# Kernel tuning notes

Hardware: AMD Instinct MI355X
Metric: run time of the kernel (lower is better)

Reference implementation:

```python
import jax, jax.numpy as jnp
import numpy as np

EPSILON = 1e-5  # parameters.EPSILON
BN_EPS = 1e-5
N_NODES, N_EDGES, D = 50000, 400000, 128


def batch_norm(x, gamma, beta):
    # BatchNorm1d in training mode: biased batch statistics over dim 0
    m = jnp.mean(x, axis=0)
    v = jnp.var(x, axis=0)
    return (x - m) * jax.lax.rsqrt(v + BN_EPS) * gamma + beta


def setup_inputs() -> dict:
    key = jax.random.key(0)
    ks = jax.random.split(key, 16)
    s = 0.05
    d = D
    inp = {
        "h": jax.random.normal(ks[0], (N_NODES, d), jnp.float32),
        "e": jax.random.normal(ks[1], (N_EDGES, d), jnp.float32),
        "src": jax.random.randint(ks[2], (N_EDGES,), 0, N_NODES, jnp.int32),
        "dst": jax.random.randint(ks[3], (N_EDGES,), 0, N_NODES, jnp.int32),
        # weights stored [in, out]
        "W_emb_node": jax.random.normal(ks[4], (d, d)) * s,
        "W_emb_edge": jax.random.normal(ks[5], (d, d)) * s,
        "W_emb_eta": jax.random.normal(ks[6], (d, d)) * s,
        "Uw": jax.random.normal(ks[7], (d, d)) * s, "Ub": jnp.zeros((d,)),
        "Vw": jax.random.normal(ks[8], (d, d)) * s, "Vb": jnp.zeros((d,)),
        "W1w": jax.random.normal(ks[9], (d, d)) * s, "W1b": jnp.zeros((d,)),
        "W2w": jax.random.normal(ks[10], (d, d)) * s, "W2b": jnp.zeros((d,)),
        "W3w": jax.random.normal(ks[11], (d, d)) * s, "W3b": jnp.zeros((d,)),
        "h_gamma": jnp.ones((d,)), "h_beta": jnp.zeros((d,)),
        "e_gamma": jnp.ones((d,)), "e_beta": jnp.zeros((d,)),
    }
    return inp


def reference(h, e, src, dst, W_emb_node, W_emb_edge, W_emb_eta,
              Uw, Ub, Vw, Vb, W1w, W1b, W2w, W2b, W3w, W3b,
              h_gamma, h_beta, e_gamma, e_beta):
    n_nodes = h.shape[0]
    # node-level linear projections
    h_emb = h @ W_emb_node                 # [N, d]
    Uh = h @ Uw + Ub                       # [N, d]
    Vh = h @ Vw + Vb                       # [N, d]
    W2h = h @ W2w + W2b                    # [N, d]
    W3h = h @ W3w + W3b                    # [N, d]
    # edge-level
    e_emb = e @ W_emb_edge                 # [E, d]
    W1e = e @ W1w + W1b                    # [E, d]
    # edge update: e_ij = emb(e) + ReLU(BN(W1 e + W2 h_src + W3 h_dst))
    pre_e = W1e + W2h[src] + W3h[dst]      # gather [E, d]
    e_new = e_emb + jax.nn.relu(batch_norm(pre_e, e_gamma, e_beta))
    # gate: sigma_ij = embedding_eta(sigmoid(e_ij))
    sigma = jax.nn.sigmoid(e_new) @ W_emb_eta  # [E, d]
    # weighted-sum aggregation to destination nodes
    num = jax.ops.segment_sum(sigma * Vh[src], dst, num_segments=n_nodes)
    den = jax.ops.segment_sum(sigma, dst, num_segments=n_nodes)
    agg = num / (den + EPSILON)            # [N, d]
    h_new = h_emb + jax.nn.relu(batch_norm(Uh + agg, h_gamma, h_beta))
    return (h_new, e_new)
```

## Files before the change

kernel.cpp:

```cpp
#include <hip/hip_runtime.h>
#include <cstdint>
#include <cstddef>
#include <cmath>

#define DD 128

typedef short bf16x8 __attribute__((ext_vector_type(8)));
typedef float f32x4 __attribute__((ext_vector_type(4)));

static __device__ __forceinline__ short f2bf(float f){
  union { float f; uint32_t u; } v; v.f = f;
  uint32_t r = v.u + 0x7FFFu + ((v.u >> 16) & 1u);
  return (short)(r >> 16);
}
static __device__ __forceinline__ float bf2f(short h){
  union { uint32_t u; float f; } v; v.u = ((uint32_t)(uint16_t)h) << 16;
  return v.f;
}
static __device__ __forceinline__ double shfl_xor_f64(double v, int m){
  long long l = __double_as_longlong(v);
  int lo = (int)(l & 0xffffffffLL);
  int hi = (int)((unsigned long long)l >> 32);
  lo = __shfl_xor(lo, m, 64);
  hi = __shfl_xor(hi, m, 64);
  return __longlong_as_double(((long long)hi << 32) | (unsigned long long)(unsigned int)lo);
}

template<int EP>
__global__ __launch_bounds__(256, 2) void fgemm_k(
    const float* __restrict__ X, const float* __restrict__ W,
    const float* __restrict__ bias, float* __restrict__ Y,
    int M, int nTiles,
    const int* __restrict__ src, const int* __restrict__ dst,
    const float* __restrict__ T2, const float* __restrict__ T3,
    double* __restrict__ eSum, double* __restrict__ eSumSq)
{
  __shared__ float sA[128][36];
  __shared__ float sW[32][128];
  __shared__ double redS[(EP == 1) ? 4 : 1][32][4];
  __shared__ double redQ[(EP == 1) ? 4 : 1][32][4];

  const int tid = threadIdx.x, tx = tid & 31, ty = tid >> 5;
  const int c0 = tx * 4, r0 = ty * 16;
  const int lane = tid & 63, wv = tid >> 6;
  const int sa_r = tid >> 1, sa_k = (tid & 1) * 16;
  const int sw_k = tid >> 3, sw_c = (tid & 7) * 16;

  float bias_c[4];
  #pragma unroll
  for (int j = 0; j < 4; ++j) bias_c[j] = bias ? bias[c0 + j] : 0.0f;

  double st_s[4] = {0,0,0,0}, st_q[4] = {0,0,0,0};

  #pragma unroll 1
  for (int tile = blockIdx.x; tile < nTiles; tile += gridDim.x){
    const int rowBase = tile * 128;
    float acc[16][4];
    #pragma unroll
    for (int r = 0; r < 16; ++r)
      #pragma unroll
      for (int j = 0; j < 4; ++j) acc[r][j] = 0.0f;

    #pragma unroll 1
    for (int h = 0; h < 4; ++h){
      {
        const float* wp = W + (size_t)(h*32 + sw_k) * DD + sw_c;
        #pragma unroll
        for (int i = 0; i < 4; ++i)
          *(f32x4*)&sW[sw_k][sw_c + i*4] = *(const f32x4*)(wp + i*4);
      }
      {
        int ar = rowBase + sa_r; if (ar >= M) ar = M - 1;
        const float* xp = X + (size_t)ar * DD + h*32 + sa_k;
        #pragma unroll
        for (int i = 0; i < 4; ++i)
          *(f32x4*)&sA[sa_r][sa_k + i*4] = *(const f32x4*)(xp + i*4);
      }
      __syncthreads();

      #pragma unroll
      for (int q = 0; q < 8; ++q){
        f32x4 b0 = *(const f32x4*)&sW[4*q + 0][c0];
        f32x4 b1 = *(const f32x4*)&sW[4*q + 1][c0];
        f32x4 b2 = *(const f32x4*)&sW[4*q + 2][c0];
        f32x4 b3 = *(const f32x4*)&sW[4*q + 3][c0];
        #pragma unroll
        for (int r = 0; r < 16; ++r){
          f32x4 a = *(const f32x4*)&sA[r0 + r][4*q];
          #pragma unroll
          for (int j = 0; j < 4; ++j){
            float t = acc[r][j];
            t = fmaf(a[0], b0[j], t); t = fmaf(a[1], b1[j], t);
            t = fmaf(a[2], b2[j], t); t = fmaf(a[3], b3[j], t);
            acc[r][j] = t;
          }
        }
      }
      __syncthreads();
    }

    #pragma unroll
    for (int r = 0; r < 16; ++r){
      int row = rowBase + r0 + r;
      if (row < M){
        size_t base = (size_t)row * DD + c0;
        if (EP == 0){
          f32x4 o;
          #pragma unroll
          for (int j = 0; j < 4; ++j) o[j] = acc[r][j] + bias_c[j];
          *(f32x4*)&Y[base] = o;
        } else {
          int s = src[row], d = dst[row];
          f32x4 t2 = *(const f32x4*)&T2[(size_t)s * DD + c0];
          f32x4 t3 = *(const f32x4*)&T3[(size_t)d * DD + c0];
          f32x4 o;
          #pragma unroll
          for (int j = 0; j < 4; ++j){
            o[j] = ((acc[r][j] + bias_c[j]) + t2[j]) + t3[j];
            st_s[j] += (double)o[j];
            st_q[j] += (double)o[j] * (double)o[j];
          }
          *(f32x4*)&Y[base] = o;
        }
      }
    }
  }

  if (EP == 1){
    #pragma unroll
    for (int j = 0; j < 4; ++j){
      st_s[j] += shfl_xor_f64(st_s[j], 32);
      st_q[j] += shfl_xor_f64(st_q[j], 32);
    }
    if (lane < 32){
      #pragma unroll
      for (int j = 0; j < 4; ++j){ redS[wv][lane][j] = st_s[j]; redQ[wv][lane][j] = st_q[j]; }
    }
    __syncthreads();
    if (tid < 128){
      int txx = tid >> 2, j = tid & 3;
      double s = 0.0, q = 0.0;
      #pragma unroll
      for (int w = 0; w < 4; ++w){ s += redS[w][txx][j]; q += redQ[w][txx][j]; }
      atomicAdd(&eSum[txx*4 + j], s);
      atomicAdd(&eSumSq[txx*4 + j], q);
    }
  }
}

__global__ __launch_bounds__(256, 2) void psgemm_k(
    const float* __restrict__ preE, const float* __restrict__ eEmb,
    const float* __restrict__ Weta,
    float* __restrict__ eNew, float* __restrict__ sigmaOut,
    const float* __restrict__ mF, const float* __restrict__ rF,
    const float* __restrict__ gF, const float* __restrict__ bF,
    int M, int nTiles)
{
  __shared__ float sA[128][36];
  __shared__ float sW[32][128];
  __shared__ float sBN[4][128];

  const int tid = threadIdx.x, tx = tid & 31, ty = tid >> 5;
  const int c0 = tx * 4, r0 = ty * 16;
  const int sa_r = tid >> 1, sa_k = (tid & 1) * 16;
  const int sw_k = tid >> 3, sw_c = (tid & 7) * 16;

  if (tid < 128){
    sBN[0][tid] = mF[tid]; sBN[1][tid] = rF[tid];
    sBN[2][tid] = gF[tid]; sBN[3][tid] = bF[tid];
  }
  __syncthreads();

  #pragma unroll 1
  for (int tile = blockIdx.x; tile < nTiles; tile += gridDim.x){
    const int rowBase = tile * 128;
    const int ar = rowBase + sa_r;

    float acc[16][4];
    #pragma unroll
    for (int r = 0; r < 16; ++r)
      #pragma unroll
      for (int j = 0; j < 4; ++j) acc[r][j] = 0.0f;

    #pragma unroll 1
    for (int h = 0; h < 4; ++h){
      {
        const float* wp = Weta + (size_t)(h*32 + sw_k) * DD + sw_c;
        #pragma unroll
        for (int i = 0; i < 4; ++i)
          *(f32x4*)&sW[sw_k][sw_c + i*4] = *(const f32x4*)(wp + i*4);
      }
      {
        int gcb = h*32 + sa_k;
        const float* pp = preE + (size_t)ar * DD + gcb;
        const float* ep = eEmb + (size_t)ar * DD + gcb;
        float* np = eNew + (size_t)ar * DD + gcb;
        #pragma unroll
        for (int i = 0; i < 4; ++i){
          f32x4 pe = *(const f32x4*)(pp + i*4);
          f32x4 em = *(const f32x4*)(ep + i*4);
          f32x4 mm = *(const f32x4*)&sBN[0][gcb + i*4];
          f32x4 rr = *(const f32x4*)&sBN[1][gcb + i*4];
          f32x4 gg = *(const f32x4*)&sBN[2][gcb + i*4];
          f32x4 bb = *(const f32x4*)&sBN[3][gcb + i*4];
          f32x4 en, sg;
          #pragma unroll
          for (int j = 0; j < 4; ++j){
            float xm  = pe[j] - mm[j];
            float t1  = xm * rr[j];
            float t2v = t1 * gg[j];
            float t3v = t2v + bb[j];
            float t = fmaxf(t3v, 0.0f);
            en[j] = em[j] + t;
            sg[j] = 1.0f / (1.0f + expf(-en[j]));
          }
          *(f32x4*)(np + i*4) = en;
          *(f32x4*)&sA[sa_r][sa_k + i*4] = sg;
        }
      }
      __syncthreads();

      #pragma unroll
      for (int q = 0; q < 8; ++q){
        f32x4 b0 = *(const f32x4*)&sW[4*q + 0][c0];
        f32x4 b1 = *(const f32x4*)&sW[4*q + 1][c0];
        f32x4 b2 = *(const f32x4*)&sW[4*q + 2][c0];
        f32x4 b3 = *(const f32x4*)&sW[4*q + 3][c0];
        #pragma unroll
        for (int r = 0; r < 16; ++r){
          f32x4 a = *(const f32x4*)&sA[r0 + r][4*q];
          #pragma unroll
          for (int j = 0; j < 4; ++j){
            float t = acc[r][j];
            t = fmaf(a[0], b0[j], t); t = fmaf(a[1], b1[j], t);
            t = fmaf(a[2], b2[j], t); t = fmaf(a[3], b3[j], t);
            acc[r][j] = t;
          }
        }
      }
      __syncthreads();
    }

    #pragma unroll
    for (int r = 0; r < 16; ++r){
      int row = rowBase + r0 + r;
      f32x4 o;
      #pragma unroll
      for (int j = 0; j < 4; ++j) o[j] = acc[r][j];
      *(f32x4*)&sigmaOut[(size_t)row * DD + c0] = o;
    }
  }
}

__global__ void hist_k(const int* __restrict__ dst, int NE, int* __restrict__ counts){
  int i = blockIdx.x * blockDim.x + threadIdx.x;
  if (i < NE) atomicAdd(&counts[dst[i]], 1);
}

__global__ __launch_bounds__(1024, 1) void scan_k(const int* __restrict__ counts, int NN,
                                                  int* __restrict__ rowStart, int* __restrict__ cursor){
  __shared__ int part[1024];
  const int T = 1024, t = threadIdx.x;
  const int chunk = (NN + T - 1) / T;
  const int lo = t * chunk;
  const int hi = (lo + chunk < NN) ? lo + chunk : NN;
  int s = 0;
  for (int i = lo; i < hi; ++i) s += counts[i];
  part[t] = s;
  __syncthreads();
  for (int off = 1; off < T; off <<= 1){
    int v = (t >= off) ? part[t - off] : 0;
    __syncthreads();
    part[t] += v;
    __syncthreads();
  }
  int run = (t == 0) ? 0 : part[t - 1];
  for (int i = lo; i < hi; ++i){ rowStart[i] = run; cursor[i] = run; run += counts[i]; }
  if (t == T - 1) rowStart[NN] = run;
}

__global__ void place_k(const int* __restrict__ dst, int NE,
                        int* __restrict__ cursor, int* __restrict__ edgeIdx){
  int i = blockIdx.x * blockDim.x + threadIdx.x;
  if (i < NE){ int p = atomicAdd(&cursor[dst[i]], 1); edgeIdx[p] = i; }
}

__global__ __launch_bounds__(256, 4) void gather_k(
    const float* __restrict__ sigma, const float* __restrict__ Vh,
    const int* __restrict__ rowStart, const int* __restrict__ edgeIdx,
    const int* __restrict__ srcArr,
    const float* __restrict__ Uh, float* __restrict__ preH, int NN)
{
  const int lane = threadIdx.x & 63, wv = threadIdx.x >> 6;
  for (int node = blockIdx.x * 4 + wv; node < NN; node += gridDim.x * 4){
    const int beg = rowStart[node], end = rowStart[node + 1];
    float den0 = 0.f, den1 = 0.f, num0 = 0.f, num1 = 0.f;
    for (int eb = beg; eb < end; eb += 8){
      const int nE = end - eb;
      float sg0[8], sg1[8], vh0[8], vh1[8];
      #pragma unroll
      for (int q = 0; q < 8; ++q){
        if (q < nE){
          int eid = edgeIdx[eb + q];
          int s = srcArr[eid];
          sg0[q] = sigma[(size_t)eid * DD + lane];
          sg1[q] = sigma[(size_t)eid * DD + 64 + lane];
          vh0[q] = Vh[(size_t)s * DD + lane];
          vh1[q] = Vh[(size_t)s * DD + 64 + lane];
        } else { sg0[q] = 0.f; sg1[q] = 0.f; vh0[q] = 0.f; vh1[q] = 0.f; }
      }
      #pragma unroll
      for (int q = 0; q < 8; ++q){
        den0 += sg0[q]; den1 += sg1[q];
        num0 = fmaf(sg0[q], vh0[q], num0);
        num1 = fmaf(sg1[q], vh1[q], num1);
      }
    }
    const size_t b = (size_t)node * DD;
    preH[b + lane]      = Uh[b + lane]      + num0 / (den0 + 1e-5f);
    preH[b + 64 + lane] = Uh[b + 64 + lane] + num1 / (den1 + 1e-5f);
  }
}

__global__ void finalizeE_k(const double* __restrict__ sum, const double* __restrict__ sumsq,
                            double M, float* __restrict__ mF, float* __restrict__ rF)
{
  int c = threadIdx.x;
  double m = sum[c] / M;
  double v = sumsq[c] / M - m * m;
  float vf = (float)v;
  mF[c] = (float)m;
  rF[c] = 1.0f / sqrtf(vf + 1e-5f);
}

__global__ void stats64_k(const float* __restrict__ X, int M,
                          double* __restrict__ sum, double* __restrict__ sumsq)
{
  const int col = threadIdx.x & 127;
  const int half = threadIdx.x >> 7;
  double s = 0.0, q = 0.0;
  for (int r = blockIdx.x * 2 + half; r < M; r += gridDim.x * 2){
    double v = (double)X[(size_t)r * DD + col];
    s += v; q += v * v;
  }
  __shared__ double sS[256], sQ[256];
  sS[threadIdx.x] = s; sQ[threadIdx.x] = q;
  __syncthreads();
  if (half == 0){
    atomicAdd(&sum[col],   sS[col] + sS[col + 128]);
    atomicAdd(&sumsq[col], sQ[col] + sQ[col + 128]);
  }
}

__global__ void finalize64_k(const double* __restrict__ sum, const double* __restrict__ sumsq,
                             double M, const float* __restrict__ gamma, const float* __restrict__ beta,
                             double* __restrict__ scale, double* __restrict__ shift)
{
  int c = threadIdx.x;
  double m = sum[c] / M;
  double var = sumsq[c] / M - m * m;
  double sc = (double)gamma[c] / sqrt(var + 1e-5);
  scale[c] = sc;
  shift[c] = (double)beta[c] - m * sc;
}

__global__ __launch_bounds__(256, 2) void hfinal_mfma_k(
    const float* __restrict__ X, const float* __restrict__ W,
    float* __restrict__ Y, int M, int rowTiles,
    const float* __restrict__ preH,
    const double* __restrict__ hSc, const double* __restrict__ hSh)
{
  const int tid = threadIdx.x;
  const int lane = tid & 63;
  const int wv = tid >> 6;
  const int l15 = lane & 15;
  const int lg = lane >> 4;
  const int colBase = blockIdx.y * 64;

  __shared__ short sW[2][64][136];
  for (int t = tid; t < 64 * 128; t += 256){
    int k = t >> 6, nl = t & 63;
    float w = W[k * DD + colBase + nl];
    short hi = f2bf(w);
    sW[0][nl][k] = hi;
    sW[1][nl][k] = f2bf(w - bf2f(hi));
  }
  __syncthreads();

  bf16x8 Bhi[4][4], Blo[4][4];
  #pragma unroll
  for (int ct = 0; ct < 4; ++ct)
    #pragma unroll
    for (int ks = 0; ks < 4; ++ks){
      Bhi[ct][ks] = *(const bf16x8*)&sW[0][ct*16 + l15][ks*32 + lg*8];
      Blo[ct][ks] = *(const bf16x8*)&sW[1][ct*16 + l15][ks*32 + lg*8];
    }

  for (int rt = blockIdx.x; rt < rowTiles; rt += gridDim.x){
    int arow = rt * 64 + wv * 16 + l15;
    if (arow >= M) arow = M - 1;
    const f32x4* xr = (const f32x4*)(X + (size_t)arow * DD);

    bf16x8 Ahi[4], Alo[4];
    #pragma unroll
    for (int ks = 0; ks < 4; ++ks){
      f32x4 a0 = xr[ks*8 + lg*2];
      f32x4 a1 = xr[ks*8 + lg*2 + 1];
      float av[8];
      #pragma unroll
      for (int j = 0; j < 4; ++j){ av[j] = a0[j]; av[4+j] = a1[j]; }
      #pragma unroll
      for (int j = 0; j < 8; ++j){
        short hi = f2bf(av[j]);
        Ahi[ks][j] = hi;
        Alo[ks][j] = f2bf(av[j] - bf2f(hi));
      }
    }

    f32x4 acc[4];
    #pragma unroll
    for (int ct = 0; ct < 4; ++ct) acc[ct] = (f32x4){0.f, 0.f, 0.f, 0.f};
    #pragma unroll
    for (int ct = 0; ct < 4; ++ct)
      #pragma unroll
      for (int ks = 0; ks < 4; ++ks){
        acc[ct] = __builtin_amdgcn_mfma_f32_16x16x32_bf16(Ahi[ks], Bhi[ct][ks], acc[ct], 0, 0, 0);
        acc[ct] = __builtin_amdgcn_mfma_f32_16x16x32_bf16(Ahi[ks], Blo[ct][ks], acc[ct], 0, 0, 0);
        acc[ct] = __builtin_amdgcn_mfma_f32_16x16x32_bf16(Alo[ks], Bhi[ct][ks], acc[ct], 0, 0, 0);
      }

    const int r0 = rt * 64 + wv * 16 + lg * 4;
    #pragma unroll
    for (int reg = 0; reg < 4; ++reg){
      int r = r0 + reg;
      if (r < M){
        #pragma unroll
        for (int ct = 0; ct < 4; ++ct){
          int c = colBase + ct*16 + l15;
          double t = (double)preH[(size_t)r * DD + c] * hSc[c] + hSh[c];
          float tv = t > 0.0 ? (float)t : 0.0f;
          Y[(size_t)r * DD + c] = acc[ct][reg] + tv;
        }
      }
    }
  }
}

extern "C" void kernel_launch(void* const* d_in, const int* in_sizes, int n_in,
                              void* d_out, int out_size, void* d_ws, size_t ws_size,
                              hipStream_t stream)
{
  const float* h  = (const float*)d_in[0];
  const float* e  = (const float*)d_in[1];
  const int* src  = (const int*)d_in[2];
  const int* dst  = (const int*)d_in[3];
  const float* Wemb_n   = (const float*)d_in[4];
  const float* Wemb_e   = (const float*)d_in[5];
  const float* Wemb_eta = (const float*)d_in[6];
  const float* Uw  = (const float*)d_in[7];  const float* Ub  = (const float*)d_in[8];
  const float* Vw  = (const float*)d_in[9];  const float* Vb  = (const float*)d_in[10];
  const float* W1w = (const float*)d_in[11]; const float* W1b = (const float*)d_in[12];
  const float* W2w = (const float*)d_in[13]; const float* W2b = (const float*)d_in[14];
  const float* W3w = (const float*)d_in[15]; const float* W3b = (const float*)d_in[16];
  const float* h_gamma = (const float*)d_in[17]; const float* h_beta = (const float*)d_in[18];
  const float* e_gamma = (const float*)d_in[19]; const float* e_beta = (const float*)d_in[20];

  const int NN = in_sizes[0] / DD;
  const int NE = in_sizes[2];

  char* wsp = (char*)d_ws;
  float* W2h    = (float*)wsp;  wsp += (size_t)NN * DD * sizeof(float);
  float* W3h    = (float*)wsp;  wsp += (size_t)NN * DD * sizeof(float);
  float* Vh     = (float*)wsp;  wsp += (size_t)NN * DD * sizeof(float);
  float* embSig = (float*)wsp;  wsp += (size_t)NE * DD * sizeof(float);
  double* stats = (double*)wsp; wsp += 6 * DD * sizeof(double);
  double* eSum = stats;        double* eSumSq = stats + DD;
  double* hSum = stats + 2*DD; double* hSumSq = stats + 3*DD;
  double* hScale = stats + 4*DD; double* hShift = stats + 5*DD;
  float* mF = (float*)wsp;   wsp += DD * sizeof(float);
  float* rF = (float*)wsp;   wsp += DD * sizeof(float);
  int* counts   = (int*)wsp; wsp += (size_t)NN * sizeof(int);
  int* rowStart = (int*)wsp; wsp += ((size_t)NN + 1) * sizeof(int);
  int* cursor   = (int*)wsp; wsp += (size_t)NN * sizeof(int);
  int* edgeIdx  = (int*)wsp; wsp += (size_t)NE * sizeof(int);

  float* h_new_out = (float*)d_out;
  float* e_out     = (float*)d_out + (size_t)NN * DD;

  const int tN = (NN + 127) / 128;
  const int tE = (NE + 127) / 128;
  const int rtN64 = (NN + 63) / 64;
  dim3 blk256(256);

  hipMemsetAsync(stats, 0, (size_t)4 * DD * sizeof(double), stream);
  hipMemsetAsync(counts, 0, (size_t)NN * sizeof(int), stream);

  hist_k<<<(NE + 255) / 256, blk256, 0, stream>>>(dst, NE, counts);
  scan_k<<<1, 1024, 0, stream>>>(counts, NN, rowStart, cursor);
  place_k<<<(NE + 255) / 256, blk256, 0, stream>>>(dst, NE, cursor, edgeIdx);

  fgemm_k<0><<<tN, blk256, 0, stream>>>(h, Uw, Ub, h_new_out, NN, tN,
      nullptr, nullptr, nullptr, nullptr, nullptr, nullptr);
  fgemm_k<0><<<tN, blk256, 0, stream>>>(h, Vw, Vb, Vh, NN, tN,
      nullptr, nullptr, nullptr, nullptr, nullptr, nullptr);
  fgemm_k<0><<<tN, blk256, 0, stream>>>(h, W2w, W2b, W2h, NN, tN,
      nullptr, nullptr, nullptr, nullptr, nullptr, nullptr);
  fgemm_k<0><<<tN, blk256, 0, stream>>>(h, W3w, W3b, W3h, NN, tN,
      nullptr, nullptr, nullptr, nullptr, nullptr, nullptr);

  fgemm_k<1><<<1024, blk256, 0, stream>>>(e, W1w, W1b, e_out, NE, tE,
      src, dst, W2h, W3h, eSum, eSumSq);

  finalizeE_k<<<1, 128, 0, stream>>>(eSum, eSumSq, (double)NE, mF, rF);

  fgemm_k<0><<<1024, blk256, 0, stream>>>(e, Wemb_e, nullptr, embSig, NE, tE,
      nullptr, nullptr, nullptr, nullptr, nullptr, nullptr);

  psgemm_k<<<1024, blk256, 0, stream>>>(e_out, embSig, Wemb_eta, e_out, embSig,
      mF, rF, e_gamma, e_beta, NE, tE);

  gather_k<<<(NN + 3) / 4, blk256, 0, stream>>>(embSig, Vh, rowStart, edgeIdx, src,
      h_new_out, h_new_out, NN);

  stats64_k<<<512, blk256, 0, stream>>>(h_new_out, NN, hSum, hSumSq);
  finalize64_k<<<1, 128, 0, stream>>>(hSum, hSumSq, (double)NN, h_gamma, h_beta, hScale, hShift);

  hfinal_mfma_k<<<dim3(rtN64, 2), blk256, 0, stream>>>(h, Wemb_n, h_new_out, NN, rtN64,
      h_new_out, hScale, hShift);
}
```

Baseline: 1.127 ms.

## Double-buffer GEMM tiles with async global-to-LDS loads

Reworks the fp32 GEMM staging into two LDS buffers with a K-step of 16. Each next tile is prefetched straight into LDS with global_load_lds while the current tile is computed, instead of loading through registers and storing. The aim is to overlap memory latency with FMAs and cut register pressure. The cost is twice as many K iterations and barriers, and an unpadded sA layout that may cause LDS bank conflicts. Correctness also depends on the barrier ordering the asynchronous LDS writes properly.

```diff
diff --git a/kernel.cpp b/kernel.cpp
--- a/kernel.cpp
+++ b/kernel.cpp
@@ -24,6 +24,12 @@
   lo = __shfl_xor(lo, m, 64);
   hi = __shfl_xor(hi, m, 64);
   return __longlong_as_double(((long long)hi << 32) | (unsigned long long)(unsigned int)lo);
+}
+
+static __device__ __forceinline__ void gl_lds16(const float* g, float* l){
+  __builtin_amdgcn_global_load_lds(
+      (const __attribute__((address_space(1))) void*)g,
+      (__attribute__((address_space(3))) void*)l, 16, 0, 0);
 }
 
 template<int EP>
@@ -35,16 +41,19 @@
     const float* __restrict__ T2, const float* __restrict__ T3,
     double* __restrict__ eSum, double* __restrict__ eSumSq)
 {
-  __shared__ float sA[128][36];
-  __shared__ float sW[32][128];
+  __shared__ float sA[2][128][16];
+  __shared__ float sW[2][16][128];
   __shared__ double redS[(EP == 1) ? 4 : 1][32][4];
   __shared__ double redQ[(EP == 1) ? 4 : 1][32][4];
 
   const int tid = threadIdx.x, tx = tid & 31, ty = tid >> 5;
   const int c0 = tx * 4, r0 = ty * 16;
   const int lane = tid & 63, wv = tid >> 6;
-  const int sa_r = tid >> 1, sa_k = (tid & 1) * 16;
-  const int sw_k = tid >> 3, sw_c = (tid & 7) * 16;
+
+  const int aRowL = wv * 32 + (lane >> 2);
+  const int aCol  = (lane & 3) * 4;
+  const int wRowL = wv * 4 + (lane >> 5);
+  const int wCol  = (lane & 31) * 4;
 
   float bias_c[4];
   #pragma unroll
@@ -55,38 +64,45 @@
   #pragma unroll 1
   for (int tile = blockIdx.x; tile < nTiles; tile += gridDim.x){
     const int rowBase = tile * 128;
+
+    {
+      #pragma unroll
+      for (int t = 0; t < 2; ++t){
+        int gr = rowBase + aRowL + t*16; if (gr >= M) gr = M - 1;
+        gl_lds16(X + (size_t)gr * DD + aCol, &sA[0][wv*32 + t*16][0]);
+        gl_lds16(W + (size_t)(wRowL + t*2) * DD + wCol, &sW[0][wv*4 + t*2][0]);
+      }
+    }
+    __syncthreads();
+
     float acc[16][4];
     #pragma unroll
     for (int r = 0; r < 16; ++r)
       #pragma unroll
       for (int j = 0; j < 4; ++j) acc[r][j] = 0.0f;
 
+    int buf = 0;
     #pragma unroll 1
-    for (int h = 0; h < 4; ++h){
-      {
-        const float* wp = W + (size_t)(h*32 + sw_k) * DD + sw_c;
+    for (int h = 0; h < 8; ++h){
+      if (h < 7){
+        const int hk = (h + 1) * 16;
         #pragma unroll
-        for (int i = 0; i < 4; ++i)
-          *(f32x4*)&sW[sw_k][sw_c + i*4] = *(const f32x4*)(wp + i*4);
-      }
-      {
-        int ar = rowBase + sa_r; if (ar >= M) ar = M - 1;
-        const float* xp = X + (size_t)ar * DD + h*32 + sa_k;
-        #pragma unroll
-        for (int i = 0; i < 4; ++i)
-          *(f32x4*)&sA[sa_r][sa_k + i*4] = *(const f32x4*)(xp + i*4);
-      }
-      __syncthreads();
-
-      #pragma unroll
-      for (int q = 0; q < 8; ++q){
-        f32x4 b0 = *(const f32x4*)&sW[4*q + 0][c0];
-        f32x4 b1 = *(const f32x4*)&sW[4*q + 1][c0];
-        f32x4 b2 = *(const f32x4*)&sW[4*q + 2][c0];
-        f32x4 b3 = *(const f32x4*)&sW[4*q + 3][c0];
+        for (int t = 0; t < 2; ++t){
+          int gr = rowBase + aRowL + t*16; if (gr >= M) gr = M - 1;
+          gl_lds16(X + (size_t)gr * DD + hk + aCol, &sA[buf^1][wv*32 + t*16][0]);
+          gl_lds16(W + (size_t)(hk + wRowL + t*2) * DD + wCol, &sW[buf^1][wv*4 + t*2][0]);
+        }
+      }
+
+      #pragma unroll
+      for (int q = 0; q < 4; ++q){
+        f32x4 b0 = *(const f32x4*)&sW[buf][4*q + 0][c0];
+        f32x4 b1 = *(const f32x4*)&sW[buf][4*q + 1][c0];
+        f32x4 b2 = *(const f32x4*)&sW[buf][4*q + 2][c0];
+        f32x4 b3 = *(const f32x4*)&sW[buf][4*q + 3][c0];
         #pragma unroll
         for (int r = 0; r < 16; ++r){
-          f32x4 a = *(const f32x4*)&sA[r0 + r][4*q];
+          f32x4 a = *(const f32x4*)&sA[buf][r0 + r][4*q];
           #pragma unroll
           for (int j = 0; j < 4; ++j){
             float t = acc[r][j];
@@ -97,6 +113,7 @@
         }
       }
       __syncthreads();
+      buf ^= 1;
     }
 
     #pragma unroll
```

Result: no change. 1.143 ms (+1.4%).
